# Kernel tuning notes

Measured on AMD Instinct MI355X. Metric: run time of the kernel, lower is better.

Reference implementation:

```python
import jax, jax.numpy as jnp
import numpy as np
from jax import lax

B, C, V, T = 8, 256, 96, 96
C8, C2 = C // 8, C // 2


def _conv3(x, w):
    # 3x3, stride 1, pad 1, no bias (the repo's misnamed 'conv1x1')
    return lax.conv_general_dilated(x, w, (1, 1), [(1, 1), (1, 1)],
                                    dimension_numbers=("NCHW", "OIHW", "NCHW"))


def _conv1(x, w, b):
    # true 1x1 conv with bias (cAttn q/k/v)
    y = lax.conv_general_dilated(x, w, (1, 1), [(0, 0), (0, 0)],
                                 dimension_numbers=("NCHW", "OIHW", "NCHW"))
    return y + b[None, :, None, None]


def setup_inputs() -> dict:
    key = jax.random.key(0)
    ks = jax.random.split(key, 20)
    s = 0.02
    d = {
        "x": jax.random.normal(ks[0], (B, C, V, T), jnp.float32),
        # vAttn (3x3 convs, no bias)
        "v_wq": jax.random.normal(ks[1], (C8, C, 3, 3), jnp.float32) * s,
        "v_wk": jax.random.normal(ks[2], (C8, C, 3, 3), jnp.float32) * s,
        "v_wv": jax.random.normal(ks[3], (C2, C, 3, 3), jnp.float32) * s,
        "v_wo": jax.random.normal(ks[4], (C, C2, 3, 3), jnp.float32) * s,
        "v_sigma": jax.random.normal(ks[5], (1,), jnp.float32),
        # tAttn
        "t_wq": jax.random.normal(ks[6], (C8, C, 3, 3), jnp.float32) * s,
        "t_wk": jax.random.normal(ks[7], (C8, C, 3, 3), jnp.float32) * s,
        "t_wv": jax.random.normal(ks[8], (C2, C, 3, 3), jnp.float32) * s,
        "t_wo": jax.random.normal(ks[9], (C, C2, 3, 3), jnp.float32) * s,
        "t_sigma": jax.random.normal(ks[10], (1,), jnp.float32),
        # cAttn (1x1 convs with bias for q/k/v, 3x3 for output proj)
        "c_wq": jax.random.normal(ks[11], (C, C, 1, 1), jnp.float32) * s,
        "c_bq": jax.random.normal(ks[12], (C,), jnp.float32) * s,
        "c_wk": jax.random.normal(ks[13], (C, C, 1, 1), jnp.float32) * s,
        "c_bk": jax.random.normal(ks[14], (C,), jnp.float32) * s,
        "c_wv": jax.random.normal(ks[15], (C, C, 1, 1), jnp.float32) * s,
        "c_bv": jax.random.normal(ks[16], (C,), jnp.float32) * s,
        "c_wo": jax.random.normal(ks[17], (C, C, 3, 3), jnp.float32) * s,
        "c_sigma": jax.random.normal(ks[18], (1,), jnp.float32),
    }
    return d


def reference(x, v_wq, v_wk, v_wv, v_wo, v_sigma,
              t_wq, t_wk, t_wv, t_wo, t_sigma,
              c_wq, c_bq, c_wk, c_bk, c_wv, c_bv, c_wo, c_sigma):
    # vAttn: attention over the v axis, independently per (b, t)
    q = _conv3(x, v_wq)                                   # [B,C8,V,T]
    k = _conv3(x, v_wk)
    v = _conv3(x, v_wv)                                   # [B,C2,V,T]
    a = jax.nn.softmax(jnp.einsum('bcvt,bcwt->btvw', q, k), axis=-1)
    av = jnp.einsum('btvw,bcwt->bcvt', a, v)              # [B,C2,V,T]
    x1 = v_sigma * _conv3(av, v_wo)

    # tAttn: attention over the t axis, independently per (b, v)
    q = _conv3(x, t_wq)
    k = _conv3(x, t_wk)
    v = _conv3(x, t_wv)
    a = jax.nn.softmax(jnp.einsum('bcvt,bcvs->bvts', q, k), axis=-1)
    av = jnp.einsum('bvts,bcvs->bcvt', a, v)
    x2 = t_sigma * _conv3(av, t_wo)

    # cAttn: attention over the channel axis, independently per (b, v)
    q = _conv1(x, c_wq, c_bq)                             # [B,C,V,T]
    k = _conv1(x, c_wk, c_bk)
    v = _conv1(x, c_wv, c_bv)
    a = jax.nn.softmax(jnp.einsum('bcvt,bdvt->bvcd', q, k), axis=-1)
    av = jnp.einsum('bvcd,bdvt->bcvt', a, v)
    x3 = c_sigma * _conv3(av, c_wo)

    return x + x1 + x2 + x3
```

## Files before the change

kernel.cpp:

```cpp
#include <hip/hip_runtime.h>
#include <math.h>

#define BB  8
#define CH  256
#define NVT 9216
#define PLN (98*98*32)
#define PROW (98*32)
#define NPK 12

typedef short bh8 __attribute__((ext_vector_type(8)));
typedef short bh4 __attribute__((ext_vector_type(4)));
typedef float f4  __attribute__((ext_vector_type(4)));

__device__ __forceinline__ float bf2f(ushort u) {
    union { uint i; float f; } x; x.i = ((uint)u) << 16; return x.f;
}
__device__ __forceinline__ ushort f2bf(float f) {
    union { float f; uint i; } x; x.f = f;
    uint r = (x.i + 0x7FFFu + ((x.i >> 16) & 1u)) >> 16;
    return (ushort)r;
}
__device__ __forceinline__ int cperm(int ci) {
    return 8 * ((ci >> 2) & 3) + 4 * (ci >> 4) + (ci & 3);
}
__device__ __forceinline__ void gld16(const void* g, void* l) {
    __builtin_amdgcn_global_load_lds(
        (const __attribute__((address_space(1))) void*)g,
        (__attribute__((address_space(3))) void*)l, 16, 0, 0);
}

struct PackArgs {
    const float* w[NPK];
    const float* scale[NPK];
    unsigned dst[NPK];
    int cin[NPK], taps[NPK], csrc[NPK], cobase[NPK], cot[NPK], kcb[NPK];
    int start[NPK + 1];
};

__global__ __launch_bounds__(256) void prep_all_k(PackArgs pa,
    ushort* __restrict__ ws, const float* __restrict__ x,
    unsigned x32_off, unsigned avl_off, unsigned b3_off,
    const float* __restrict__ bq, const float* __restrict__ bk,
    const float* __restrict__ bv, int packBlocks)
{
    const int bid = blockIdx.x;
    const int tid = threadIdx.x;

    if (bid < 192) {
        int p = bid;
        ushort* base = (p < 64) ? ws + x32_off + (size_t)p * PLN
                                : ws + avl_off + (size_t)(p - 64) * PLN;
        const bh8 z = {0,0,0,0,0,0,0,0};
        for (int n = tid; n < 1552; n += 256) {
            size_t off;
            if (n < 392)       off = (size_t)n * 8;
            else if (n < 784)  off = (size_t)97 * PROW + (size_t)(n - 392) * 8;
            else {
                int m = n - 784;
                int vq = m >> 3, side = (m >> 2) & 1, sub = m & 3;
                off = ((size_t)(vq + 1) * 98 + side * 97) * 32 + sub * 8;
            }
            *(bh8*)&base[off] = z;
        }
        return;
    }
    if (bid < 195) {
        int i = (bid - 192) * 256 + tid;
        if (i < 768) {
            float* o = (float*)(ws + b3_off);
            o[i] = (i < 256) ? bq[i] : (i < 512 ? bk[i - 256] : bv[i - 512]);
        }
        return;
    }
    if (bid < 195 + packBlocks) {
        int n = (bid - 195) * 256 + tid;
        if (n >= pa.start[NPK]) return;
        int s = 0;
#pragma unroll
        for (int k = 1; k < NPK; ++k) if (n >= pa.start[k]) s = k;
        int m   = n - pa.start[s];
        int kl  = m & 31;
        int rem = m >> 5;
        int col = rem % pa.csrc[s]; rem /= pa.csrc[s];
        int tap = rem % pa.taps[s];
        int kc  = rem / pa.taps[s];
        int ci  = kc * 32 + kl;
        int g   = (kl >> 2) & 3;
        int i   = ((kl >> 4) << 2) | (kl & 3);
        int cog = pa.cobase[s] + col;
        int cot = cog >> 4, lc = cog & 15;
        float v = pa.w[s][((size_t)col * pa.cin[s] + ci) * pa.taps[s] + tap];
        if (pa.scale[s]) v *= pa.scale[s][0];
        ws[pa.dst[s] +
           ((((size_t)(pa.kcb[s] + kc) * pa.taps[s] + tap) * pa.cot[s] + cot) * 64
            + (g * 16 + lc)) * 8 + i] = f2bf(v);
        return;
    }

    __shared__ ushort tile[96 * 32];
    int cvb = bid - (195 + packBlocks);
    int v = cvb % 96, kc = (cvb / 96) & 7, b = cvb / 768;
    int ci = tid >> 3, tp = tid & 7;
    const float* src = x + (((size_t)(b * 256 + kc * 32 + ci)) * 96 + v) * 96 + tp * 12;
    int pc = cperm(ci);
    int gci = pc >> 3, idx = pc & 7;
#pragma unroll
    for (int u = 0; u < 12; ++u) {
        int t = tp * 12 + u;
        int sw = ((t + 1) >> 1) & 3;
        tile[t * 32 + 8 * (gci ^ sw) + idx] = f2bf(src[u]);
    }
    __syncthreads();
    ushort* dst = ws + x32_off + (((size_t)(b * 8 + kc) * 98 + v + 1) * 98 + 1) * 32;
    for (int n = tid; n < 384; n += 256)
        *(bh8*)&dst[n * 8] = *(const bh8*)&tile[n * 8];
}

template<int TAPS, int CT, int OMODE, int KU, int NWC>
__global__ __launch_bounds__(512, 2) void conv_mfma(
    const ushort* __restrict__ xin, const ushort* __restrict__ wpk,
    ushort* __restrict__ obf, ushort* __restrict__ aux,
    float* __restrict__ oacc, const float* __restrict__ bias, int KC)
{
    constexpr int ROWS  = (TAPS == 9) ? 3 : 1;
    constexpr int CH1   = (ROWS * PROW * 2 + 1023) / 1024;
    constexpr int CHUNKS = KU * CH1;
    constexpr int BUFSZ = CHUNKS * 512;
    constexpr int COT   = NWC * CT;
    constexpr int COUT  = COT * 16;
    constexpr int NT    = (NWC == 8) ? 6 : 3;
    __shared__ ushort sx[2][BUFSZ];

    const int v0 = blockIdx.x, b = blockIdx.y;
    const int tid = threadIdx.x;
    const int w = tid >> 6, l = tid & 63;
    const int g = l >> 4, lc = l & 15;
    const int wc = w % NWC, sub = w / NWC;
    const int tbase = (NWC == 4) ? sub * 48 : 0;

    f4 acc[CT][NT];
#pragma unroll
    for (int ct = 0; ct < CT; ++ct)
#pragma unroll
        for (int nt = 0; nt < NT; ++nt) acc[ct][nt] = (f4){0.f, 0.f, 0.f, 0.f};

    const bh8* wp0 = (const bh8*)wpk + (size_t)(wc * CT) * 64 + l;

    auto stage = [&](int kcp, int buf) {
#pragma unroll
        for (int u = 0; u < KU; ++u) {
            const ushort* src = xin +
                (((size_t)b * KC + kcp * KU + u) * 98 + v0
                 + ((TAPS == 9) ? 0 : 1)) * (size_t)PROW;
#pragma unroll
            for (int c = 0; c < (CH1 + 7) / 8; ++c) {
                int ch = w + c * 8;
                if (ch < CH1)
                    gld16(src + ch * 512 + l * 8,
                          &sx[buf][(u * CH1 + ch) * 512 + l * 8]);
            }
        }
    };

    stage(0, 0);
    __syncthreads();
    const int NP = KC / KU;
    for (int kcp = 0; kcp < NP; ++kcp) {
        const int cur = kcp & 1;
        if (kcp + 1 < NP) stage(kcp + 1, cur ^ 1);
#pragma unroll
        for (int u = 0; u < KU; ++u) {
            const int kc = kcp * KU + u;
#pragma unroll
            for (int tap = 0; tap < TAPS; ++tap) {
                const int kh = (TAPS == 9) ? tap / 3 : 0;
                const int kw = (TAPS == 9) ? tap % 3 : 1;
                bh8 af[CT];
#pragma unroll
                for (int ct = 0; ct < CT; ++ct)
                    af[ct] = wp0[(((size_t)kc * TAPS + tap) * COT + ct) * 64];
#pragma unroll
                for (int nt = 0; nt < NT; ++nt) {
                    int tp = tbase + nt * 16 + lc + kw;
                    bh8 bf = *(const bh8*)&sx[cur][u * CH1 * 512 + kh * PROW
                                                   + tp * 32
                                                   + 8 * (g ^ ((tp >> 1) & 3))];
#pragma unroll
                    for (int ct = 0; ct < CT; ++ct)
                        acc[ct][nt] = __builtin_amdgcn_mfma_f32_16x16x32_bf16(
                            af[ct], bf, acc[ct][nt], 0, 0, 0);
                }
            }
        }
        __syncthreads();
    }

#pragma unroll
    for (int ct = 0; ct < CT; ++ct) {
#pragma unroll
        for (int nt = 0; nt < NT; ++nt) {
            int tt = tbase + nt * 16 + lc;
            if (OMODE == 0) {
#pragma unroll
                for (int j = 0; j < 4; ++j) {
                    int cog = (wc * CT + ct) * 16 + g * 4 + j;
                    float val = acc[ct][nt][j];
                    if (bias) val += bias[cog];
                    obf[(((size_t)b * COUT + cog) * 96 + v0) * 96 + tt] = f2bf(val);
                }
            } else if (OMODE == 6) {
                int cogb = (wc * CT + ct) * 16;
                if (cogb < 512) {
#pragma unroll
                    for (int j = 0; j < 4; ++j) {
                        int cog = cogb + g * 4 + j;
                        float val = acc[ct][nt][j] + bias[cog];
                        obf[(((size_t)b * 512 + cog) * 96 + v0) * 96 + tt] = f2bf(val);
                    }
                } else {
                    bh4 o;
#pragma unroll
                    for (int j = 0; j < 4; ++j)
                        o[j] = (short)f2bf(acc[ct][nt][j] + bias[cogb + g * 4 + j]);
                    *(bh4*)&aux[(((size_t)b * 96 + v0) * 96 + tt) * 256
                                + (cogb - 512) + g * 4] = o;
                }
            } else {
                int cb  = (wc * CT + ct) * 16 + g * 4;
                int ci5 = cb & 31;
                int gci = (ci5 >> 2) & 3;
                int idx = 4 * (ci5 >> 4);
                int swr = ((1 + tt) >> 1) & 3;
                const ushort* xr = aux +
                    ((((size_t)b * 8 + (cb >> 5)) * 98 + 1 + v0) * 98 + 1 + tt) * 32;
                bh4 rvv = *(const bh4*)&xr[8 * (gci ^ swr) + idx];
#pragma unroll
                for (int j = 0; j < 4; ++j) {
                    size_t o = (((size_t)b * 256 + cb + j) * 96 + v0) * 96 + tt;
                    oacc[o] = bf2f((ushort)rvv[j]) + acc[ct][nt][j];
                }
            }
        }
    }
}

__global__ __launch_bounds__(256) void transpose_vt_k(const ushort* __restrict__ in,
                                                      ushort* __restrict__ out,
                                                      int cs_in, int cn)
{
    __shared__ ushort tile[96][100];
    int b = blockIdx.x / cn, c = blockIdx.x % cn;
    size_t sbase = ((size_t)b * cs_in + c) * NVT;
    size_t dbase = (size_t)blockIdx.x * NVT;
    for (int n = threadIdx.x; n < NVT; n += 256) tile[n / 96][n % 96] = in[sbase + n];
    __syncthreads();
    for (int n = threadIdx.x; n < NVT; n += 256) out[dbase + n] = tile[n % 96][n / 96];
}

template<bool OVER_V>
__global__ __launch_bounds__(384) void attn_vt_mfma_k(const ushort* __restrict__ qkv,
                                                      ushort* __restrict__ avall,
                                                      int sec, int cstride, int cbase)
{
    __shared__ ushort sQT[96 * 40];
    __shared__ ushort sKT[96 * 40];
    __shared__ ushort sV[128 * 104];

    int b = blockIdx.x / 96, p = blockIdx.x % 96;
    int tid = threadIdx.x;
    int wv = tid >> 6, l = tid & 63;
    int g = l >> 4, lc = l & 15;

    const size_t base = ((size_t)b * cstride + cbase) * (size_t)NVT + (size_t)p * 96;

    for (int s = tid; s < 768; s += 384) {
        int hf = s / 384;
        int c  = (s % 384) / 12;
        int m  = s % 12;
        bh8 val = *(const bh8*)&qkv[base + (size_t)(hf * 32 + c) * NVT + 8 * m];
        ushort* dst = hf ? sKT : sQT;
#pragma unroll
        for (int u = 0; u < 8; ++u)
            dst[(8 * m + u) * 40 + c] = (ushort)val[u];
    }
    for (int s = tid; s < 1536; s += 384) {
        int c = s / 12, m = s % 12;
        *(bh8*)&sV[c * 104 + 8 * m] =
            *(const bh8*)&qkv[base + (size_t)(64 + c) * NVT + 8 * m];
    }
    __syncthreads();

    bh4 qlo = *(const bh4*)&sQT[(wv * 16 + lc) * 40 + 4 * g];
    bh4 qhi = *(const bh4*)&sQT[(wv * 16 + lc) * 40 + 4 * g + 16];
    bh8 bq = __builtin_shufflevector(qlo, qhi, 0, 1, 2, 3, 4, 5, 6, 7);

    f4 st[6];
#pragma unroll
    for (int mt = 0; mt < 6; ++mt) {
        bh4 alo = *(const bh4*)&sKT[(mt * 16 + lc) * 40 + 4 * g];
        bh4 ahi = *(const bh4*)&sKT[(mt * 16 + lc) * 40 + 4 * g + 16];
        bh8 ak = __builtin_shufflevector(alo, ahi, 0, 1, 2, 3, 4, 5, 6, 7);
        st[mt] = __builtin_amdgcn_mfma_f32_16x16x32_bf16(ak, bq,
                                                         (f4){0.f, 0.f, 0.f, 0.f},
                                                         0, 0, 0);
    }

    float mx = -1e30f;
#pragma unroll
    for (int mt = 0; mt < 6; ++mt)
#pragma unroll
        for (int j = 0; j < 4; ++j) mx = fmaxf(mx, st[mt][j]);
    mx = fmaxf(mx, __shfl_xor(mx, 16));
    mx = fmaxf(mx, __shfl_xor(mx, 32));
    float sum = 0.f;
#pragma unroll
    for (int mt = 0; mt < 6; ++mt)
#pragma unroll
        for (int j = 0; j < 4; ++j) {
            float e = __expf(st[mt][j] - mx);
            st[mt][j] = e;
            sum += e;
        }
    sum += __shfl_xor(sum, 16);
    sum += __shfl_xor(sum, 32);
    float inv = 1.f / sum;

    bh8 pf[3];
#pragma unroll
    for (int ks = 0; ks < 3; ++ks) {
        bh8 t;
#pragma unroll
        for (int i = 0; i < 8; ++i)
            t[i] = (short)f2bf(st[2 * ks + (i >> 2)][i & 3] * inv);
        pf[ks] = t;
    }

    f4 acc[8];
#pragma unroll
    for (int mt = 0; mt < 8; ++mt) acc[mt] = (f4){0.f, 0.f, 0.f, 0.f};
#pragma unroll
    for (int ks = 0; ks < 3; ++ks)
#pragma unroll
        for (int mt = 0; mt < 8; ++mt) {
            bh4 alo = *(const bh4*)&sV[(mt * 16 + lc) * 104 + ks * 32 + 4 * g];
            bh4 ahi = *(const bh4*)&sV[(mt * 16 + lc) * 104 + ks * 32 + 4 * g + 16];
            bh8 avf = __builtin_shufflevector(alo, ahi, 0, 1, 2, 3, 4, 5, 6, 7);
            acc[mt] = __builtin_amdgcn_mfma_f32_16x16x32_bf16(avf, pf[ks],
                                                              acc[mt], 0, 0, 0);
        }

    int i = wv * 16 + lc;
#pragma unroll
    for (int mt = 0; mt < 8; ++mt) {
        int vv_ = OVER_V ? i : p;
        int tt_ = OVER_V ? p : i;
        int sw  = ((1 + tt_) >> 1) & 3;
        bh4 o;
#pragma unroll
        for (int j = 0; j < 4; ++j) o[j] = (short)f2bf(acc[mt][j]);
        size_t off = ((((size_t)b * 16 + sec + (mt >> 1)) * 98 + 1 + vv_) * 98
                      + 1 + tt_) * 32 + 8 * (g ^ sw) + 4 * (mt & 1);
        *(bh4*)&avall[off] = o;
    }
}

__global__ __launch_bounds__(256) void attn_c_k(const ushort* __restrict__ qkc,
    const ushort* __restrict__ vc, ushort* __restrict__ avall)
{
    __shared__ ushort sQ[64 * 104];
    __shared__ ushort sK[256 * 104];
    __shared__ ushort sV[96 * 264];
    __shared__ ushort sP[64 * 264];

    int v = blockIdx.x, cc = blockIdx.y, b = blockIdx.z;
    int c0 = cc * 64;
    int tid = threadIdx.x;
    int w = tid >> 6, l = tid & 63;
    int g = l >> 4, lc = l & 15;

    for (int s = tid; s < 64 * 12; s += 256) {
        int r = s / 12, sg = s % 12;
        *(bh8*)&sQ[r * 104 + sg * 8] =
            *(const bh8*)&qkc[(((size_t)b * 512 + c0 + r) * 96 + v) * 96 + sg * 8];
    }
    for (int s = tid; s < 256 * 12; s += 256) {
        int r = s / 12, sg = s % 12;
        *(bh8*)&sK[r * 104 + sg * 8] =
            *(const bh8*)&qkc[(((size_t)b * 512 + 256 + r) * 96 + v) * 96 + sg * 8];
    }
    for (int s = tid; s < 96 * 32; s += 256) {
        int r = s / 32, sg = s % 32;
        *(bh8*)&sV[r * 264 + sg * 8] =
            *(const bh8*)&vc[(((size_t)b * 96 + v) * 96 + r) * 256 + sg * 8];
    }
    __syncthreads();

    f4 s16[16];
#pragma unroll
    for (int nt = 0; nt < 16; ++nt) s16[nt] = (f4){0.f, 0.f, 0.f, 0.f};
#pragma unroll
    for (int ks = 0; ks < 3; ++ks) {
        bh4 alo = *(const bh4*)&sQ[(w * 16 + lc) * 104 + ks * 32 + 4 * g];
        bh4 ahi = *(const bh4*)&sQ[(w * 16 + lc) * 104 + ks * 32 + 4 * g + 16];
        bh8 aq = __builtin_shufflevector(alo, ahi, 0, 1, 2, 3, 4, 5, 6, 7);
#pragma unroll
        for (int nt = 0; nt < 16; ++nt) {
            bh4 blo = *(const bh4*)&sK[(nt * 16 + lc) * 104 + ks * 32 + 4 * g];
            bh4 bhi = *(const bh4*)&sK[(nt * 16 + lc) * 104 + ks * 32 + 4 * g + 16];
            bh8 bk = __builtin_shufflevector(blo, bhi, 0, 1, 2, 3, 4, 5, 6, 7);
            s16[nt] = __builtin_amdgcn_mfma_f32_16x16x32_bf16(aq, bk, s16[nt], 0, 0, 0);
        }
    }
#pragma unroll
    for (int j = 0; j < 4; ++j) {
        float m = -1e30f;
#pragma unroll
        for (int nt = 0; nt < 16; ++nt) m = fmaxf(m, s16[nt][j]);
        m = fmaxf(m, __shfl_xor(m, 1));
        m = fmaxf(m, __shfl_xor(m, 2));
        m = fmaxf(m, __shfl_xor(m, 4));
        m = fmaxf(m, __shfl_xor(m, 8));
        float sum = 0.f;
#pragma unroll
        for (int nt = 0; nt < 16; ++nt) {
            float e = __expf(s16[nt][j] - m); s16[nt][j] = e; sum += e;
        }
        sum += __shfl_xor(sum, 1);
        sum += __shfl_xor(sum, 2);
        sum += __shfl_xor(sum, 4);
        sum += __shfl_xor(sum, 8);
        float inv = 1.f / sum;
#pragma unroll
        for (int nt = 0; nt < 16; ++nt)
            sP[(w * 16 + g * 4 + j) * 264 + nt * 16 + lc] = f2bf(s16[nt][j] * inv);
    }
    __syncthreads();

    f4 o6[6];
#pragma unroll
    for (int nt = 0; nt < 6; ++nt) o6[nt] = (f4){0.f, 0.f, 0.f, 0.f};
#pragma unroll
    for (int ks = 0; ks < 8; ++ks) {
        bh4 alo = *(const bh4*)&sP[(w * 16 + lc) * 264 + ks * 32 + 4 * g];
        bh4 ahi = *(const bh4*)&sP[(w * 16 + lc) * 264 + ks * 32 + 4 * g + 16];
        bh8 ap = __builtin_shufflevector(alo, ahi, 0, 1, 2, 3, 4, 5, 6, 7);
#pragma unroll
        for (int nt = 0; nt < 6; ++nt) {
            bh4 blo = *(const bh4*)&sV[(nt * 16 + lc) * 264 + ks * 32 + 4 * g];
            bh4 bhi = *(const bh4*)&sV[(nt * 16 + lc) * 264 + ks * 32 + 4 * g + 16];
            bh8 bv = __builtin_shufflevector(blo, bhi, 0, 1, 2, 3, 4, 5, 6, 7);
            o6[nt] = __builtin_amdgcn_mfma_f32_16x16x32_bf16(ap, bv, o6[nt], 0, 0, 0);
        }
    }
#pragma unroll
    for (int nt = 0; nt < 6; ++nt) {
        int t = nt * 16 + lc;
        int sw = ((1 + t) >> 1) & 3;
        bh4 o;
#pragma unroll
        for (int j = 0; j < 4; ++j) o[j] = (short)f2bf(o6[nt][j]);
        size_t off = ((((size_t)b * 16 + 8 + cc * 2 + (w >> 1)) * 98 + 1 + v) * 98
                      + 1 + t) * 32 + 8 * (g ^ sw) + 4 * (w & 1);
        *(bh4*)&avall[off] = o;
    }
}

extern "C" void kernel_launch(void* const* d_in, const int* in_sizes, int n_in,
                              void* d_out, int out_size, void* d_ws, size_t ws_size,
                              hipStream_t stream)
{
    const float* x     = (const float*)d_in[0];
    const float* v_wq  = (const float*)d_in[1];
    const float* v_wk  = (const float*)d_in[2];
    const float* v_wv  = (const float*)d_in[3];
    const float* v_wo  = (const float*)d_in[4];
    const float* v_sig = (const float*)d_in[5];
    const float* t_wq  = (const float*)d_in[6];
    const float* t_wk  = (const float*)d_in[7];
    const float* t_wv  = (const float*)d_in[8];
    const float* t_wo  = (const float*)d_in[9];
    const float* t_sig = (const float*)d_in[10];
    const float* c_wq  = (const float*)d_in[11];
    const float* c_bq  = (const float*)d_in[12];
    const float* c_wk  = (const float*)d_in[13];
    const float* c_bk  = (const float*)d_in[14];
    const float* c_wv  = (const float*)d_in[15];
    const float* c_bv  = (const float*)d_in[16];
    const float* c_wo  = (const float*)d_in[17];
    const float* c_sig = (const float*)d_in[18];

    float*  out = (float*)d_out;
    ushort* ws  = (ushort*)d_ws;

    const size_t X32  = 0;
    const size_t AVL  = X32 + 19685376;
    const size_t POOL = AVL + 39354368;
    const size_t QKV   = POOL;
    const size_t QKVVT = POOL + 28311552;
    const size_t QKC   = POOL;
    const size_t VCT   = POOL + 37748736;
    const size_t PK    = POOL + 56623104;
    const size_t PK_PVT = PK;
    const size_t PK_C3  = PK_PVT + 884736;
    const size_t PK_FIN = PK_C3 + 196608;
    const size_t B3     = PK_FIN + 1179648;

    PackArgs pa;
    auto setp = [&](int s, const float* w, size_t dst, int cin, int taps,
                    int csrc, int cobase, int cot, int kcb, const float* sc) {
        pa.w[s] = w; pa.scale[s] = sc; pa.dst[s] = (unsigned)dst;
        pa.cin[s] = cin; pa.taps[s] = taps; pa.csrc[s] = csrc;
        pa.cobase[s] = cobase; pa.cot[s] = cot; pa.kcb[s] = kcb;
    };
    setp(0,  v_wq, PK_PVT, 256, 9, 32, 0, 24, 0, nullptr);
    setp(1,  v_wk, PK_PVT, 256, 9, 32, 32, 24, 0, nullptr);
    setp(2,  v_wv, PK_PVT, 256, 9, 128, 64, 24, 0, nullptr);
    setp(3,  t_wq, PK_PVT, 256, 9, 32, 192, 24, 0, nullptr);
    setp(4,  t_wk, PK_PVT, 256, 9, 32, 224, 24, 0, nullptr);
    setp(5,  t_wv, PK_PVT, 256, 9, 128, 256, 24, 0, nullptr);
    setp(6,  c_wq, PK_C3, 256, 1, 256, 0, 48, 0, nullptr);
    setp(7,  c_wk, PK_C3, 256, 1, 256, 256, 48, 0, nullptr);
    setp(8,  c_wv, PK_C3, 256, 1, 256, 512, 48, 0, nullptr);
    setp(9,  v_wo, PK_FIN, 128, 9, 256, 0, 16, 0, v_sig);
    setp(10, t_wo, PK_FIN, 128, 9, 256, 0, 16, 4, t_sig);
    setp(11, c_wo, PK_FIN, 256, 9, 256, 0, 16, 8, c_sig);
    pa.start[0] = 0;
    for (int s = 0; s < NPK; ++s)
        pa.start[s + 1] = pa.start[s]
            + (pa.cin[s] >> 5) * pa.taps[s] * pa.csrc[s] * 32;
    const int packBlocks = (pa.start[NPK] + 255) / 256;
    const int totalBlocks = 195 + packBlocks + 96 * 8 * BB;
    prep_all_k<<<totalBlocks, 256, 0, stream>>>(pa, ws, x,
        (unsigned)X32, (unsigned)AVL, (unsigned)B3, c_bq, c_bk, c_bv, packBlocks);

    conv_mfma<9, 6, 0, 2, 4><<<dim3(96, BB), 512, 0, stream>>>(
        ws + X32, ws + PK_PVT, ws + QKV, nullptr, nullptr, nullptr, 8);

    transpose_vt_k<<<BB * 192, 256, 0, stream>>>(ws + QKV, ws + QKVVT, 384, 192);
    attn_vt_mfma_k<true><<<BB * 96, 384, 0, stream>>>(ws + QKVVT, ws + AVL, 0, 192, 0);

    attn_vt_mfma_k<false><<<BB * 96, 384, 0, stream>>>(ws + QKV, ws + AVL, 4, 384, 192);

    conv_mfma<1, 6, 6, 4, 8><<<dim3(96, BB), 512, 0, stream>>>(
        ws + X32, ws + PK_C3, ws + QKC, ws + VCT, nullptr,
        (const float*)(ws + B3), 8);
    attn_c_k<<<dim3(96, 4, BB), 256, 0, stream>>>(ws + QKC, ws + VCT, ws + AVL);

    conv_mfma<9, 4, 5, 2, 4><<<dim3(96, BB), 512, 0, stream>>>(
        ws + AVL, ws + PK_FIN, nullptr, ws + X32, out, nullptr, 16);
}
```

Baseline: 596.3 us.

## Add software-pipelined final conv kernel and merge the two axis-attention launches

Adds a dedicated final 3x3 conv kernel that triple-buffers input channel chunks in LDS through async global-to-LDS loads. Weight fragments are double-buffered in registers and the next chunk is staged while MFMAs run on the current one, which is meant to hide load latency behind compute. The residual add and fp32 output moves into this kernel's epilogue. It also merges the V-axis and T-axis attention launches into one 2D grid with a runtime branch, cutting one launch and letting the two halves run concurrently. The cost is more register pressure from holding two sets of weight fragments, and the attention kernel loses its compile-time OVER_V specialisation.

```diff
diff --git a/kernel.cpp b/kernel.cpp
--- a/kernel.cpp
+++ b/kernel.cpp
@@ -208,7 +208,7 @@
                     if (bias) val += bias[cog];
                     obf[(((size_t)b * COUT + cog) * 96 + v0) * 96 + tt] = f2bf(val);
                 }
-            } else if (OMODE == 6) {
+            } else {
                 int cogb = (wc * CT + ct) * 16;
                 if (cogb < 512) {
 #pragma unroll
@@ -225,20 +225,135 @@
                     *(bh4*)&aux[(((size_t)b * 96 + v0) * 96 + tt) * 256
                                 + (cogb - 512) + g * 4] = o;
                 }
-            } else {
-                int cb  = (wc * CT + ct) * 16 + g * 4;
-                int ci5 = cb & 31;
-                int gci = (ci5 >> 2) & 3;
-                int idx = 4 * (ci5 >> 4);
-                int swr = ((1 + tt) >> 1) & 3;
-                const ushort* xr = aux +
-                    ((((size_t)b * 8 + (cb >> 5)) * 98 + 1 + v0) * 98 + 1 + tt) * 32;
-                bh4 rvv = *(const bh4*)&xr[8 * (gci ^ swr) + idx];
-#pragma unroll
-                for (int j = 0; j < 4; ++j) {
-                    size_t o = (((size_t)b * 256 + cb + j) * 96 + v0) * 96 + tt;
-                    oacc[o] = bf2f((ushort)rvv[j]) + acc[ct][nt][j];
-                }
+            }
+        }
+    }
+}
+
+__global__ __launch_bounds__(512) void conv_fin_pipe(
+    const ushort* __restrict__ xin, const ushort* __restrict__ wpk,
+    const ushort* __restrict__ xres32, float* __restrict__ oacc, int KC)
+{
+    constexpr int CH1 = 19;
+    constexpr int CT  = 2;
+    constexpr int COT = 16;
+    constexpr int NT  = 6;
+    __shared__ ushort sx[3][CH1 * 512];
+
+    const int v0 = blockIdx.x, b = blockIdx.y;
+    const int tid = threadIdx.x;
+    const int w = tid >> 6, l = tid & 63;
+    const int g = l >> 4, lc = l & 15;
+    const int wc = w;
+
+    f4 acc[CT][NT];
+#pragma unroll
+    for (int ct = 0; ct < CT; ++ct)
+#pragma unroll
+        for (int nt = 0; nt < NT; ++nt) acc[ct][nt] = (f4){0.f, 0.f, 0.f, 0.f};
+
+    const bh8* wp0 = (const bh8*)wpk + (size_t)(wc * CT) * 64 + l;
+
+    auto stage = [&](int kc, int buf) {
+        const ushort* src = xin + (((size_t)b * KC + kc) * 98 + v0) * (size_t)PROW;
+#pragma unroll
+        for (int c = 0; c < 3; ++c) {
+            int ch = w + c * 8;
+            if (ch < CH1)
+                gld16(src + ch * 512 + l * 8, &sx[buf][ch * 512 + l * 8]);
+        }
+    };
+    bh8 wfA[9][CT], wfB[9][CT];
+    auto ldwA = [&](int kc) {
+#pragma unroll
+        for (int tap = 0; tap < 9; ++tap)
+#pragma unroll
+            for (int ct = 0; ct < CT; ++ct)
+                wfA[tap][ct] = wp0[(((size_t)kc * 9 + tap) * COT + ct) * 64];
+    };
+    auto ldwB = [&](int kc) {
+#pragma unroll
+        for (int tap = 0; tap < 9; ++tap)
+#pragma unroll
+            for (int ct = 0; ct < CT; ++ct)
+                wfB[tap][ct] = wp0[(((size_t)kc * 9 + tap) * COT + ct) * 64];
+    };
+    auto bodyA = [&](int t) {
+        const ushort* bp = sx[t % 3];
+#pragma unroll
+        for (int tap = 0; tap < 9; ++tap) {
+            const int kh = tap / 3, kw = tap % 3;
+#pragma unroll
+            for (int nt = 0; nt < NT; ++nt) {
+                int tp = nt * 16 + lc + kw;
+                bh8 bf = *(const bh8*)&bp[kh * PROW + tp * 32
+                                          + 8 * (g ^ ((tp >> 1) & 3))];
+#pragma unroll
+                for (int ct = 0; ct < CT; ++ct)
+                    acc[ct][nt] = __builtin_amdgcn_mfma_f32_16x16x32_bf16(
+                        wfA[tap][ct], bf, acc[ct][nt], 0, 0, 0);
+            }
+        }
+    };
+    auto bodyB = [&](int t) {
+        const ushort* bp = sx[t % 3];
+#pragma unroll
+        for (int tap = 0; tap < 9; ++tap) {
+            const int kh = tap / 3, kw = tap % 3;
+#pragma unroll
+            for (int nt = 0; nt < NT; ++nt) {
+                int tp = nt * 16 + lc + kw;
+                bh8 bf = *(const bh8*)&bp[kh * PROW + tp * 32
+                                          + 8 * (g ^ ((tp >> 1) & 3))];
+#pragma unroll
+                for (int ct = 0; ct < CT; ++ct)
+                    acc[ct][nt] = __builtin_amdgcn_mfma_f32_16x16x32_bf16(
+                        wfB[tap][ct], bf, acc[ct][nt], 0, 0, 0);
+            }
+        }
+    };
+
+    stage(0, 0);
+    stage(1, 1);
+    ldwA(0);
+    asm volatile("s_waitcnt vmcnt(0)" ::: "memory");
+    __builtin_amdgcn_s_barrier();
+    __builtin_amdgcn_sched_barrier(0);
+
+    for (int t = 0; t < KC; t += 2) {
+        if (t) {
+            __builtin_amdgcn_s_barrier();
+            __builtin_amdgcn_sched_barrier(0);
+        }
+        if (t + 2 < KC) stage(t + 2, (t + 2) % 3);
+        if (t + 1 < KC) ldwB(t + 1);
+        bodyA(t);
+        if (t + 1 < KC) {
+            __builtin_amdgcn_s_barrier();
+            __builtin_amdgcn_sched_barrier(0);
+            if (t + 3 < KC) stage(t + 3, (t + 3) % 3);
+            if (t + 2 < KC) ldwA(t + 2);
+            bodyB(t + 1);
+        }
+    }
+
+#pragma unroll
+    for (int ct = 0; ct < CT; ++ct) {
+#pragma unroll
+        for (int nt = 0; nt < NT; ++nt) {
+            int tt = nt * 16 + lc;
+            int cb  = (wc * CT + ct) * 16 + g * 4;
+            int ci5 = cb & 31;
+            int gci = (ci5 >> 2) & 3;
+            int idx = 4 * (ci5 >> 4);
+            int swr = ((1 + tt) >> 1) & 3;
+            const ushort* xr = xres32 +
+                ((((size_t)b * 8 + (cb >> 5)) * 98 + 1 + v0) * 98 + 1 + tt) * 32;
+            bh4 rvv = *(const bh4*)&xr[8 * (gci ^ swr) + idx];
+#pragma unroll
+            for (int j = 0; j < 4; ++j) {
+                size_t o = (((size_t)b * 256 + cb + j) * 96 + v0) * 96 + tt;
+                oacc[o] = bf2f((ushort)rvv[j]) + acc[ct][nt][j];
             }
         }
     }
@@ -257,14 +372,19 @@
     for (int n = threadIdx.x; n < NVT; n += 256) out[dbase + n] = tile[n % 96][n / 96];
 }
 
-template<bool OVER_V>
-__global__ __launch_bounds__(384) void attn_vt_mfma_k(const ushort* __restrict__ qkv,
-                                                      ushort* __restrict__ avall,
-                                                      int sec, int cstride, int cbase)
+__global__ __launch_bounds__(384) void attn_vt_mfma_k(const ushort* __restrict__ qkvA,
+                                                      const ushort* __restrict__ qkvB,
+                                                      ushort* __restrict__ avall)
 {
     __shared__ ushort sQT[96 * 40];
     __shared__ ushort sKT[96 * 40];
     __shared__ ushort sV[128 * 104];
+
+    const bool over_v = (blockIdx.y == 0);
+    const ushort* qkv = over_v ? qkvA : qkvB;
+    const int cstride = over_v ? 192 : 384;
+    const int cbase   = over_v ? 0 : 192;
+    const int sec     = over_v ? 0 : 4;
 
     int b = blockIdx.x / 96, p = blockIdx.x % 96;
     int tid = threadIdx.x;
@@ -352,8 +472,8 @@
     int i = wv * 16 + lc;
 #pragma unroll
     for (int mt = 0; mt < 8; ++mt) {
-        int vv_ = OVER_V ? i : p;
-        int tt_ = OVER_V ? p : i;
+        int vv_ = over_v ? i : p;
+        int tt_ = over_v ? p : i;
         int sw  = ((1 + tt_) >> 1) & 3;
         bh4 o;
 #pragma unroll
@@ -537,15 +657,14 @@
         ws + X32, ws + PK_PVT, ws + QKV, nullptr, nullptr, nullptr, 8);
 
     transpose_vt_k<<<BB * 192, 256, 0, stream>>>(ws + QKV, ws + QKVVT, 384, 192);
-    attn_vt_mfma_k<true><<<BB * 96, 384, 0, stream>>>(ws + QKVVT, ws + AVL, 0, 192, 0);
-
-    attn_vt_mfma_k<false><<<BB * 96, 384, 0, stream>>>(ws + QKV, ws + AVL, 4, 384, 192);
+    attn_vt_mfma_k<<<dim3(BB * 96, 2), 384, 0, stream>>>(ws + QKVVT, ws + QKV,
+                                                         ws + AVL);
 
     conv_mfma<1, 6, 6, 4, 8><<<dim3(96, BB), 512, 0, stream>>>(
         ws + X32, ws + PK_C3, ws + QKC, ws + VCT, nullptr,
         (const float*)(ws + B3), 8);
     attn_c_k<<<dim3(96, 4, BB), 256, 0, stream>>>(ws + QKC, ws + VCT, ws + AVL);
 
-    conv_mfma<9, 4, 5, 2, 4><<<dim3(96, BB), 512, 0, stream>>>(
-        ws + AVL, ws + PK_FIN, nullptr, ws + X32, out, nullptr, 16);
-}
+    conv_fin_pipe<<<dim3(96, BB), 512, 0, stream>>>(
+        ws + AVL, ws + PK_FIN, ws + X32, out, 16);
+}
```

Result: slower. 635.6 us (+6.6%).
